# Performance work log

Measured on AMD Instinct MI355X. Metric: run time of the kernel, lower is better.

## Reference

```python
import jax, jax.numpy as jnp
import numpy as np

BN_EPS = 1e-5


def _bn(y, g, b, m, v):
    # BatchNorm1d in eval mode (running stats), faithful to torch's affine BN
    return (y - m) * jax.lax.rsqrt(v + BN_EPS) * g + b


def setup_inputs() -> dict:
    key = jax.random.key(0)
    ks = jax.random.split(key, 6)
    N, E, C_IN, C_OUT = 20000, 640000, 128, 256
    x = jax.random.normal(ks[0], (N, C_IN), dtype=jnp.float32)
    tpl_edge_index = jax.random.randint(ks[1], (2, E), 0, N, dtype=jnp.int64)
    def lin(k, o, i):
        return jax.random.normal(k, (o, i), dtype=jnp.float32) * 0.05
    inp = {
        'x': x,
        'tpl_edge_index': tpl_edge_index,
        'W1': lin(ks[2], C_OUT, 2 * C_IN), 'b1': jnp.zeros((C_OUT,), jnp.float32),
        'g1': jnp.ones((C_OUT,), jnp.float32), 'be1': jnp.zeros((C_OUT,), jnp.float32),
        'm1': jnp.zeros((C_OUT,), jnp.float32), 'v1': jnp.ones((C_OUT,), jnp.float32),
        'W2': lin(ks[3], C_OUT, C_OUT), 'b2': jnp.zeros((C_OUT,), jnp.float32),
        'g2': jnp.ones((C_OUT,), jnp.float32), 'be2': jnp.zeros((C_OUT,), jnp.float32),
        'm2': jnp.zeros((C_OUT,), jnp.float32), 'v2': jnp.ones((C_OUT,), jnp.float32),
        'W3': lin(ks[4], C_OUT, C_OUT), 'b3': jnp.zeros((C_OUT,), jnp.float32),
        'g3': jnp.ones((C_OUT,), jnp.float32), 'be3': jnp.zeros((C_OUT,), jnp.float32),
        'm3': jnp.zeros((C_OUT,), jnp.float32), 'v3': jnp.ones((C_OUT,), jnp.float32),
    }
    return inp


def reference(x, tpl_edge_index, W1, b1, g1, be1, m1, v1,
              W2, b2, g2, be2, m2, v2, W3, b3, g3, be3, m3, v3):
    N = x.shape[0]
    # remove_self_loops + add_self_loops: under max aggregation, duplicate
    # self-loop messages (x_j - x_i == 0) are idempotent, so appending one
    # self-loop per node is mathematically identical.
    loops = jnp.arange(N, dtype=tpl_edge_index.dtype)
    src = jnp.concatenate([tpl_edge_index[0], loops])  # x_j indices
    tgt = jnp.concatenate([tpl_edge_index[1], loops])  # x_i / aggregation indices
    x_i = x[tgt]                                       # [E+N, C_in]
    x_j = x[src]
    h = jnp.concatenate([x_i, x_j - x_i], axis=1)      # [E+N, 2*C_in]
    h = _bn(jax.nn.relu(h @ W1.T + b1), g1, be1, m1, v1)
    h = _bn(jax.nn.relu(h @ W2.T + b2), g2, be2, m2, v2)
    agg = jax.ops.segment_max(h, tgt, num_segments=N)  # scatter-max -> [N, C_out]
    out = _bn(jax.nn.relu(agg @ W3.T + b3), g3, be3, m3, v3)
    return out
```

## Files before the change

### kernel.cpp

```cpp
#include <hip/hip_runtime.h>
#include <stdint.h>

#define BN_EPS 1e-5f

typedef __bf16 bf16x8 __attribute__((ext_vector_type(8)));
typedef __bf16 bf16x2 __attribute__((ext_vector_type(2)));
typedef float  f32x4  __attribute__((ext_vector_type(4)));
typedef float  f32x2  __attribute__((ext_vector_type(2)));

__device__ __forceinline__ unsigned short f2bf(float f) {
    unsigned u = __float_as_uint(f);
    unsigned r = (u + 0x7FFFu + ((u >> 16) & 1u)) >> 16;
    return (unsigned short)r;
}
__device__ __forceinline__ unsigned pkb(float a, float b) {
    f32x2 f; f.x = a; f.y = b;
    bf16x2 h = __builtin_convertvector(f, bf16x2);
    return *(unsigned*)&h;
}
__device__ __forceinline__ unsigned ar2(unsigned p, unsigned q) {
    f32x2 a, b;
    a.x = __uint_as_float(p << 16);
    a.y = __uint_as_float(p & 0xFFFF0000u);
    b.x = __uint_as_float(q << 16);
    b.y = __uint_as_float(q & 0xFFFF0000u);
    f32x2 s = a + b;
    return pkb(fmaxf(s.x, 0.f), fmaxf(s.y, 0.f));
}
__device__ __forceinline__ int swz(int row, int k) {
    const int blk = k >> 3;
    const int sb = (blk & 24) | ((blk ^ row) & 7);
    return (row << 8) + (sb << 3) + (k & 7);
}
__device__ __forceinline__ int swz128(int row, int k) {
    const int blk = k >> 3;
    const int sb = (blk & 8) | ((blk ^ row) & 7);
    return (row << 7) + (sb << 3) + (k & 7);
}

__global__ void prep_kernel(
    const int* __restrict__ eidx,
    int E, int M,
    const float* __restrict__ W1, const float* __restrict__ W2, const float* __restrict__ W3,
    const float* __restrict__ b1, const float* __restrict__ g1, const float* __restrict__ be1,
    const float* __restrict__ m1, const float* __restrict__ v1,
    const float* __restrict__ b2, const float* __restrict__ g2, const float* __restrict__ be2,
    const float* __restrict__ m2, const float* __restrict__ v2,
    const float* __restrict__ b3, const float* __restrict__ g3, const float* __restrict__ be3,
    const float* __restrict__ m3, const float* __restrict__ v3,
    unsigned short* __restrict__ W1b, unsigned short* __restrict__ W2b,
    unsigned short* __restrict__ W3b, float* __restrict__ consts,
    unsigned* __restrict__ mask2, unsigned* __restrict__ count)
{
    const int idx = blockIdx.x * 256 + threadIdx.x;
    if (idx < 65536) {
        const int row = idx >> 8, c = idx & 255;
        float w1v = (c < 128) ? (W1[row * 256 + c] - W1[row * 256 + c + 128])
                              : W1[row * 256 + c];
        W1b[idx] = f2bf(w1v);
        const float s1c = g1[c] * rsqrtf(v1[c] + BN_EPS);
        W2b[idx] = f2bf(W2[idx] * s1c);
        const float s2c = g2[c] * rsqrtf(v2[c] + BN_EPS);
        W3b[idx] = f2bf(W3[idx] * s2c);
    }
    if (idx < 128) {
        const float sa = g2[2 * idx]     * rsqrtf(v2[2 * idx]     + BN_EPS);
        const float sb = g2[2 * idx + 1] * rsqrtf(v2[2 * idx + 1] + BN_EPS);
        mask2[idx] = (sa < 0.f ? 0xFFFFu : 0u) | ((sb < 0.f ? 0xFFFFu : 0u) << 16);
    }
    if (idx < 768) {
        const int l = idx >> 8, c = idx & 255;
        const float* bp  = l == 0 ? b1  : (l == 1 ? b2  : b3);
        const float* gp  = l == 0 ? g1  : (l == 1 ? g2  : g3);
        const float* bep = l == 0 ? be1 : (l == 1 ? be2 : be3);
        const float* mp  = l == 0 ? m1  : (l == 1 ? m2  : m3);
        const float* vp  = l == 0 ? v1  : (l == 1 ? v2  : v3);
        const float s = gp[c] * rsqrtf(vp[c] + BN_EPS);
        consts[l * 768 + c]       = bp[c];
        consts[l * 768 + 256 + c] = s;
        consts[l * 768 + 512 + c] = bep[c] - mp[c] * s;
    }
    if (idx < M) {
        const int tgt = (idx < E) ? eidx[E + idx] : (idx - E);
        atomicAdd(&count[tgt], 1u);
    }
}

__global__ __launch_bounds__(1024) void scan_matvec_kernel(
    const unsigned* __restrict__ count, unsigned* __restrict__ cursor, int N,
    const float* __restrict__ W2, const float* __restrict__ W3,
    float* __restrict__ consts)
{
    const int t = threadIdx.x;
    if (blockIdx.x > 0) {
        const int g = (blockIdx.x - 1) * 16 + (t >> 6);
        const int lane = t & 63;
        const int l = g >> 8, c = g & 255;
        const float* W = l ? W3 : W2;
        const float* tv = consts + (l ? (768 + 512) : 512);
        float4 w4 = *(const float4*)&W[c * 256 + lane * 4];
        float4 t4 = *(const float4*)&tv[lane * 4];
        float s = w4.x * t4.x + w4.y * t4.y + w4.z * t4.z + w4.w * t4.w;
        #pragma unroll
        for (int d = 1; d < 64; d <<= 1) s += __shfl_xor(s, d);
        if (lane == 0) consts[(l ? 1536 : 768) + c] += s;
        return;
    }
    __shared__ unsigned part[1024];
    const int per = (N + 1023) / 1024;
    const int b = t * per;
    unsigned s = 0;
    if (b + per <= N && (per & 3) == 0) {
        for (int i = 0; i < per; i += 4) {
            uint4 c4 = *(const uint4*)(count + b + i);
            s += c4.x + c4.y + c4.z + c4.w;
        }
    } else {
        for (int i = 0; i < per; i++) if (b + i < N) s += count[b + i];
    }
    part[t] = s;
    __syncthreads();
    for (int off = 1; off < 1024; off <<= 1) {
        unsigned v = (t >= off) ? part[t - off] : 0u;
        __syncthreads();
        part[t] += v;
        __syncthreads();
    }
    unsigned run = (t > 0) ? part[t - 1] : 0u;
    for (int i = 0; i < per; i++) {
        if (b + i < N) {
            unsigned c = count[b + i];
            cursor[b + i] = run;
            run += c;
        }
    }
}

__global__ __launch_bounds__(512) void scatpq_kernel(
    const int* __restrict__ eidx, int E, int M, int nScat,
    unsigned* __restrict__ cursor, int* __restrict__ spair,
    const float* __restrict__ x, int N,
    const unsigned short* __restrict__ W1b,
    const float* __restrict__ consts,
    unsigned short* __restrict__ Pb, unsigned short* __restrict__ Qb)
{
    __shared__ unsigned short Xs[64 * 128];
    const int t = threadIdx.x;

    if ((int)blockIdx.x < nScat) {
        const int i = blockIdx.x * 512 + t;
        if (i < M) {
            int s, tg;
            if (i < E) { s = eidx[i]; tg = eidx[E + i]; }
            else       { s = tg = i - E; }
            const unsigned pos = atomicAdd(&cursor[tg], 1u);
            int2* p = (int2*)spair;
            p[pos] = make_int2(s, tg);
        }
        return;
    }

    const int base = (blockIdx.x - nScat) * 64;
    {
        const int row = t >> 3, part = t & 7;
        const int node = base + row;
        const int c0 = part * 16;
        if (node < N) {
            const float* s = x + (size_t)node * 128 + c0;
            float4 a0 = *(const float4*)(s);
            float4 a1 = *(const float4*)(s + 4);
            float4 a2 = *(const float4*)(s + 8);
            float4 a3 = *(const float4*)(s + 12);
            uint4 p0 = {pkb(a0.x, a0.y), pkb(a0.z, a0.w), pkb(a1.x, a1.y), pkb(a1.z, a1.w)};
            uint4 p1 = {pkb(a2.x, a2.y), pkb(a2.z, a2.w), pkb(a3.x, a3.y), pkb(a3.z, a3.w)};
            *(uint4*)&Xs[swz128(row, c0)]     = p0;
            *(uint4*)&Xs[swz128(row, c0 + 8)] = p1;
        } else {
            const uint4 z = {0u, 0u, 0u, 0u};
            *(uint4*)&Xs[swz128(row, c0)]     = z;
            *(uint4*)&Xs[swz128(row, c0 + 8)] = z;
        }
    }
    __syncthreads();

    const int lane = t & 63;
    const int wv   = t >> 6;
    const int n16  = lane & 15;
    const int qd   = lane >> 4;
    const int wc   = wv * 32;

    const f32x4 vzero = {0.f, 0.f, 0.f, 0.f};

    #pragma unroll
    for (int ph = 0; ph < 2; ph++) {
        f32x4 acc[2][4];
        #pragma unroll
        for (int i = 0; i < 2; i++)
            #pragma unroll
            for (int j = 0; j < 4; j++) acc[i][j] = vzero;

        #pragma unroll
        for (int ks = 0; ks < 4; ks++) {
            const int k0 = ks * 32 + qd * 8;
            bf16x8 a[2], b[4];
            #pragma unroll
            for (int ci = 0; ci < 2; ci++)
                a[ci] = *(const bf16x8*)&W1b[(size_t)(wc + ci * 16 + n16) * 256 + ph * 128 + k0];
            #pragma unroll
            for (int rj = 0; rj < 4; rj++)
                b[rj] = *(const bf16x8*)&Xs[swz128(rj * 16 + n16, k0)];
            #pragma unroll
            for (int ci = 0; ci < 2; ci++)
                #pragma unroll
                for (int rj = 0; rj < 4; rj++)
                    acc[ci][rj] = __builtin_amdgcn_mfma_f32_16x16x32_bf16(a[ci], b[rj], acc[ci][rj], 0, 0, 0);
        }

        unsigned short* dst = ph == 0 ? Pb : Qb;
        #pragma unroll
        for (int ci = 0; ci < 2; ci++) {
            const int col0 = wc + ci * 16 + qd * 4;
            float4 bb = {0.f, 0.f, 0.f, 0.f};
            if (ph == 0) bb = *(const float4*)&consts[col0];
            #pragma unroll
            for (int rj = 0; rj < 4; rj++) {
                const int node = base + rj * 16 + n16;
                if (node < N) {
                    uint2 p = {pkb(acc[ci][rj][0] + bb.x, acc[ci][rj][1] + bb.y),
                               pkb(acc[ci][rj][2] + bb.z, acc[ci][rj][3] + bb.w)};
                    *(uint2*)(dst + (size_t)node * 256 + col0) = p;
                }
            }
        }
    }
}

__global__ __launch_bounds__(512) void msg_kernel(
    const unsigned short* __restrict__ Pb,
    const unsigned short* __restrict__ Qb,
    const int* __restrict__ spair,
    int M, int chunk,
    const unsigned short* __restrict__ W2b,
    const float* __restrict__ consts,
    const unsigned* __restrict__ mask2,
    unsigned* __restrict__ agg)
{
    __shared__ unsigned short At[64 * 256];
    __shared__ int tgt_l[64];

    const int tile = (blockIdx.x & 7) * chunk + (blockIdx.x >> 3);
    if (tile * 64 >= M) return;
    const int base = tile * 64;
    const int t = threadIdx.x;

    {
        const int row = t >> 3, part = t & 7;
        const int slot = base + row;
        const int c0 = part * 32;
        if (slot < M) {
            const int2 pr = *(const int2*)(spair + 2 * slot);
            if (part == 0) tgt_l[row] = pr.y;
            const unsigned short* Pp = Pb + (size_t)pr.y * 256 + c0;
            const unsigned short* Qp = Qb + (size_t)pr.x * 256 + c0;
            uint4 P4[4], Q4[4];
            #pragma unroll
            for (int w = 0; w < 4; w++) P4[w] = *(const uint4*)(Pp + w * 8);
            #pragma unroll
            for (int w = 0; w < 4; w++) Q4[w] = *(const uint4*)(Qp + w * 8);
            #pragma unroll
            for (int w = 0; w < 4; w++) {
                uint4 u;
                u.x = ar2(P4[w].x, Q4[w].x);
                u.y = ar2(P4[w].y, Q4[w].y);
                u.z = ar2(P4[w].z, Q4[w].z);
                u.w = ar2(P4[w].w, Q4[w].w);
                *(uint4*)&At[swz(row, c0 + w * 8)] = u;
            }
        } else {
            if (part == 0) tgt_l[row] = -1;
            const uint4 z = {0u, 0u, 0u, 0u};
            #pragma unroll
            for (int w = 0; w < 4; w++) *(uint4*)&At[swz(row, c0 + w * 8)] = z;
        }
    }
    __syncthreads();

    const int lane = t & 63;
    const int wv   = t >> 6;
    const int n16  = lane & 15;
    const int qd   = lane >> 4;
    const int wc   = wv * 32;

    const f32x4 vzero = {0.f, 0.f, 0.f, 0.f};
    f32x4 acc[2][4];
    #pragma unroll
    for (int i = 0; i < 2; i++)
        #pragma unroll
        for (int j = 0; j < 4; j++) acc[i][j] = vzero;

    #pragma unroll
    for (int ks = 0; ks < 8; ks++) {
        const int k0 = ks * 32 + qd * 8;
        bf16x8 a[2], b[4];
        #pragma unroll
        for (int ci = 0; ci < 2; ci++)
            a[ci] = *(const bf16x8*)&W2b[(size_t)(wc + ci * 16 + n16) * 256 + k0];
        #pragma unroll
        for (int rj = 0; rj < 4; rj++)
            b[rj] = *(const bf16x8*)&At[swz(rj * 16 + n16, k0)];
        #pragma unroll
        for (int ci = 0; ci < 2; ci++)
            #pragma unroll
            for (int rj = 0; rj < 4; rj++)
                acc[ci][rj] = __builtin_amdgcn_mfma_f32_16x16x32_bf16(a[ci], b[rj], acc[ci][rj], 0, 0, 0);
    }
    __syncthreads();

    {
        const float* B2 = consts + 768;
        #pragma unroll
        for (int ci = 0; ci < 2; ci++) {
            const int col0 = wc + ci * 16 + qd * 4;
            const float4 bb = *(const float4*)&B2[col0];
            const uint2 mk = *(const uint2*)&mask2[col0 >> 1];
            #pragma unroll
            for (int rj = 0; rj < 4; rj++) {
                const int row = rj * 16 + n16;
                float r0 = fmaxf(acc[ci][rj][0] + bb.x, 0.f);
                float r1 = fmaxf(acc[ci][rj][1] + bb.y, 0.f);
                float r2 = fmaxf(acc[ci][rj][2] + bb.z, 0.f);
                float r3 = fmaxf(acc[ci][rj][3] + bb.w, 0.f);
                uint2 p = {pkb(r0, r1) ^ mk.x, pkb(r2, r3) ^ mk.y};
                *(uint2*)&At[swz(row, col0)] = p;
            }
        }
    }
    __syncthreads();

    {
        const int r0 = (wv & 3) * 16;
        const int cb = (wv >> 2) * 128 + lane * 2;
        const int myt = (lane < 16) ? tgt_l[r0 + lane] : -1;
        int curT = -1;
        unsigned m0 = 0, m1 = 0;
        for (int r = 0; r < 16; r++) {
            const int tg = __shfl(myt, r);
            const unsigned k2 = *(const unsigned*)&At[swz(r0 + r, cb)];
            const unsigned k0 = k2 & 0xFFFFu, k1 = k2 >> 16;
            if (tg != curT) {
                if (curT >= 0) {
                    unsigned* p = &agg[(size_t)curT * 256 + cb];
                    atomicMax(p, m0); atomicMax(p + 1, m1);
                }
                curT = tg; m0 = k0; m1 = k1;
            } else {
                m0 = m0 > k0 ? m0 : k0;
                m1 = m1 > k1 ? m1 : k1;
            }
        }
        if (curT >= 0) {
            unsigned* p = &agg[(size_t)curT * 256 + cb];
            atomicMax(p, m0); atomicMax(p + 1, m1);
        }
    }
}

__global__ __launch_bounds__(256) void out_kernel(
    const unsigned* __restrict__ agg, int N,
    const unsigned short* __restrict__ W3b,
    const float* __restrict__ consts,
    const unsigned* __restrict__ mask2,
    float* __restrict__ out)
{
    __shared__ unsigned short At[32 * 256];

    const int t = threadIdx.x;
    const int base = blockIdx.x * 32;

    {
        const int row = t >> 3, part = t & 7;
        const int node = base + row;
        const int c0 = part * 32;
        if (node < N) {
            const unsigned* ap = agg + (size_t)node * 256 + c0;
            #pragma unroll
            for (int w = 0; w < 4; w++) {
                uint4 a = *(const uint4*)(ap + w * 8);
                uint4 b = *(const uint4*)(ap + w * 8 + 4);
                const uint4 mk = *(const uint4*)&mask2[(c0 + w * 8) >> 1];
                uint4 p;
                p.x = (a.x | (a.y << 16)) ^ mk.x;
                p.y = (a.z | (a.w << 16)) ^ mk.y;
                p.z = (b.x | (b.y << 16)) ^ mk.z;
                p.w = (b.z | (b.w << 16)) ^ mk.w;
                *(uint4*)&At[swz(row, c0 + w * 8)] = p;
            }
        } else {
            const uint4 z = {0u, 0u, 0u, 0u};
            #pragma unroll
            for (int w = 0; w < 4; w++) *(uint4*)&At[swz(row, c0 + w * 8)] = z;
        }
    }
    __syncthreads();

    const int lane = t & 63;
    const int wv   = t >> 6;
    const int n16  = lane & 15;
    const int qd   = lane >> 4;
    const int wc   = wv * 64;

    const f32x4 vzero = {0.f, 0.f, 0.f, 0.f};
    f32x4 acc[2][4];
    #pragma unroll
    for (int i = 0; i < 2; i++)
        #pragma unroll
        for (int j = 0; j < 4; j++) acc[i][j] = vzero;

    #pragma unroll
    for (int ks = 0; ks < 8; ks++) {
        const int k0 = ks * 32 + qd * 8;
        bf16x8 a[2];
        #pragma unroll
        for (int ri = 0; ri < 2; ri++)
            a[ri] = *(const bf16x8*)&At[swz(ri * 16 + n16, k0)];
        #pragma unroll
        for (int ci = 0; ci < 4; ci++) {
            bf16x8 b = *(const bf16x8*)&W3b[(size_t)(wc + ci * 16 + n16) * 256 + k0];
            #pragma unroll
            for (int ri = 0; ri < 2; ri++)
                acc[ri][ci] = __builtin_amdgcn_mfma_f32_16x16x32_bf16(a[ri], b, acc[ri][ci], 0, 0, 0);
        }
    }

    {
        const float* B3 = consts + 1536;
        const float* S3 = consts + 1536 + 256;
        const float* T3 = consts + 1536 + 512;
        #pragma unroll
        for (int ci = 0; ci < 4; ci++) {
            const int col = wc + ci * 16 + n16;
            const float bb = B3[col], ss = S3[col], tt = T3[col];
            #pragma unroll
            for (int ri = 0; ri < 2; ri++) {
                #pragma unroll
                for (int r = 0; r < 4; r++) {
                    const int row = ri * 16 + qd * 4 + r;
                    const int node = base + row;
                    if (node < N) {
                        float v = fmaxf(acc[ri][ci][r] + bb, 0.f) * ss + tt;
                        out[(size_t)node * 256 + col] = v;
                    }
                }
            }
        }
    }
}

extern "C" void kernel_launch(void* const* d_in, const int* in_sizes, int n_in,
                              void* d_out, int out_size, void* d_ws, size_t ws_size,
                              hipStream_t stream)
{
    const float* x  = (const float*)d_in[0];
    const int* eidx = (const int*)d_in[1];
    const int N = in_sizes[0] / 128;
    const int E = in_sizes[1] / 2;
    const int M = E + N;
    const int nTiles = (M + 63) / 64;
    const int chunk = (nTiles + 7) / 8;
    const int nScat = (M + 511) / 512;
    const int nPQ = (N + 63) / 64;

    char* ws = (char*)d_ws;
    unsigned short* W1b = (unsigned short*)(ws);
    unsigned short* W2b = (unsigned short*)(ws + 131072);
    unsigned short* W3b = (unsigned short*)(ws + 262144);
    float* consts       = (float*)(ws + 393216);
    unsigned* mask2     = (unsigned*)(ws + 402432);
    size_t off = 402944;
    unsigned* agg       = (unsigned*)(ws + off);       off += (size_t)N * 256 * 4;
    unsigned* count     = (unsigned*)(ws + off);       off += (size_t)N * 4;
    unsigned* cursor    = (unsigned*)(ws + off);       off += (size_t)N * 4;
    int* spair          = (int*)(ws + off);            off += (size_t)M * 8;
    unsigned short* Pb  = (unsigned short*)(ws + off); off += (size_t)N * 256 * 2;
    unsigned short* Qb  = (unsigned short*)(ws + off);

    hipMemsetAsync(agg, 0, (size_t)N * 256 * 4, stream);
    hipMemsetAsync(count, 0, (size_t)N * 4, stream);

    int work = M;
    if (65536 > work) work = 65536;
    hipLaunchKernelGGL(prep_kernel, dim3((work + 255) / 256), dim3(256), 0, stream,
        eidx, E, M,
        (const float*)d_in[2], (const float*)d_in[8], (const float*)d_in[14],
        (const float*)d_in[3], (const float*)d_in[4], (const float*)d_in[5],
        (const float*)d_in[6], (const float*)d_in[7],
        (const float*)d_in[9], (const float*)d_in[10], (const float*)d_in[11],
        (const float*)d_in[12], (const float*)d_in[13],
        (const float*)d_in[15], (const float*)d_in[16], (const float*)d_in[17],
        (const float*)d_in[18], (const float*)d_in[19],
        W1b, W2b, W3b, consts, mask2, count);

    hipLaunchKernelGGL(scan_matvec_kernel, dim3(33), dim3(1024), 0, stream,
        count, cursor, N,
        (const float*)d_in[8], (const float*)d_in[14], consts);

    hipLaunchKernelGGL(scatpq_kernel, dim3(nScat + nPQ), dim3(512), 0, stream,
        eidx, E, M, nScat, cursor, spair,
        x, N, W1b, consts, Pb, Qb);

    hipLaunchKernelGGL(msg_kernel, dim3(chunk * 8), dim3(512), 0, stream,
        Pb, Qb, spair, M, chunk, W2b, consts, mask2, agg);

    hipLaunchKernelGGL(out_kernel, dim3((N + 31) / 32), dim3(256), 0, stream,
        agg, N, W3b, consts, mask2, (float*)d_out);
}
```

Baseline: 471.6 us.

## Use per-wave LDS epilogue tiles to drop block barriers; fold agg zeroing into prep

The msg_kernel epilogue now writes each wave's 64x32 output slice into a private swizzled LDS buffer and performs the segment-max scan on that slice itself, removing two block-wide __syncthreads. Each lane handles one column pair across 16 rows, with four row groups per wave. Zeroing of the aggregation buffer moves from a separate hipMemsetAsync into a grid-stride loop inside prep_kernel, saving one launch. The costs are about 32KB of extra LDS per block, which may lower occupancy, and a different atomic pattern: runs break per quarter-wave, so more atomics may be issued.

```diff
diff --git a/kernel.cpp b/kernel.cpp
--- a/kernel.cpp
+++ b/kernel.cpp
@@ -36,6 +36,10 @@
     const int blk = k >> 3;
     const int sb = (blk & 8) | ((blk ^ row) & 7);
     return (row << 7) + (sb << 3) + (k & 7);
+}
+__device__ __forceinline__ int swz32(int row, int c) {
+    const int cc = c ^ (((row ^ (row >> 3)) & 7) << 2);
+    return (row << 5) + cc;
 }
 
 __global__ void prep_kernel(
@@ -50,7 +54,8 @@
     const float* __restrict__ m3, const float* __restrict__ v3,
     unsigned short* __restrict__ W1b, unsigned short* __restrict__ W2b,
     unsigned short* __restrict__ W3b, float* __restrict__ consts,
-    unsigned* __restrict__ mask2, unsigned* __restrict__ count)
+    unsigned* __restrict__ mask2, unsigned* __restrict__ count,
+    unsigned* __restrict__ agg, int aggWords)
 {
     const int idx = blockIdx.x * 256 + threadIdx.x;
     if (idx < 65536) {
@@ -83,6 +88,12 @@
     if (idx < M) {
         const int tgt = (idx < E) ? eidx[E + idx] : (idx - E);
         atomicAdd(&count[tgt], 1u);
+    }
+    {
+        const uint4 z = {0u, 0u, 0u, 0u};
+        const int stride = gridDim.x * 256 * 4;
+        for (int i = idx * 4; i < aggWords; i += stride)
+            *(uint4*)&agg[i] = z;
     }
 }
 
@@ -246,6 +257,7 @@
     unsigned* __restrict__ agg)
 {
     __shared__ unsigned short At[64 * 256];
+    __shared__ unsigned short Kt[8][64 * 32];
     __shared__ int tgt_l[64];
 
     const int tile = (blockIdx.x & 7) * chunk + (blockIdx.x >> 3);
@@ -314,13 +326,14 @@
             for (int rj = 0; rj < 4; rj++)
                 acc[ci][rj] = __builtin_amdgcn_mfma_f32_16x16x32_bf16(a[ci], b[rj], acc[ci][rj], 0, 0, 0);
     }
-    __syncthreads();
-
+
+    unsigned short* K = Kt[wv];
     {
         const float* B2 = consts + 768;
         #pragma unroll
         for (int ci = 0; ci < 2; ci++) {
-            const int col0 = wc + ci * 16 + qd * 4;
+            const int cl = ci * 16 + qd * 4;
+            const int col0 = wc + cl;
             const float4 bb = *(const float4*)&B2[col0];
             const uint2 mk = *(const uint2*)&mask2[col0 >> 1];
             #pragma unroll
@@ -331,25 +344,25 @@
                 float r2 = fmaxf(acc[ci][rj][2] + bb.z, 0.f);
                 float r3 = fmaxf(acc[ci][rj][3] + bb.w, 0.f);
                 uint2 p = {pkb(r0, r1) ^ mk.x, pkb(r2, r3) ^ mk.y};
-                *(uint2*)&At[swz(row, col0)] = p;
+                *(uint2*)&K[swz32(row, cl)] = p;
             }
         }
     }
-    __syncthreads();
-
-    {
-        const int r0 = (wv & 3) * 16;
-        const int cb = (wv >> 2) * 128 + lane * 2;
-        const int myt = (lane < 16) ? tgt_l[r0 + lane] : -1;
+
+    {
+        const int cp = lane & 15;
+        const int q  = lane >> 4;
+        const int myt = tgt_l[lane];
         int curT = -1;
         unsigned m0 = 0, m1 = 0;
-        for (int r = 0; r < 16; r++) {
-            const int tg = __shfl(myt, r);
-            const unsigned k2 = *(const unsigned*)&At[swz(r0 + r, cb)];
+        for (int j = 0; j < 16; j++) {
+            const int row = q * 16 + j;
+            const int tg = __shfl(myt, row);
+            const unsigned k2 = *(const unsigned*)&K[swz32(row, cp * 2)];
             const unsigned k0 = k2 & 0xFFFFu, k1 = k2 >> 16;
             if (tg != curT) {
                 if (curT >= 0) {
-                    unsigned* p = &agg[(size_t)curT * 256 + cb];
+                    unsigned* p = &agg[(size_t)curT * 256 + wc + cp * 2];
                     atomicMax(p, m0); atomicMax(p + 1, m1);
                 }
                 curT = tg; m0 = k0; m1 = k1;
@@ -359,7 +372,7 @@
             }
         }
         if (curT >= 0) {
-            unsigned* p = &agg[(size_t)curT * 256 + cb];
+            unsigned* p = &agg[(size_t)curT * 256 + wc + cp * 2];
             atomicMax(p, m0); atomicMax(p + 1, m1);
         }
     }
@@ -484,7 +497,6 @@
     unsigned short* Pb  = (unsigned short*)(ws + off); off += (size_t)N * 256 * 2;
     unsigned short* Qb  = (unsigned short*)(ws + off);
 
-    hipMemsetAsync(agg, 0, (size_t)N * 256 * 4, stream);
     hipMemsetAsync(count, 0, (size_t)N * 4, stream);
 
     int work = M;
@@ -498,7 +510,7 @@
         (const float*)d_in[12], (const float*)d_in[13],
         (const float*)d_in[15], (const float*)d_in[16], (const float*)d_in[17],
         (const float*)d_in[18], (const float*)d_in[19],
-        W1b, W2b, W3b, consts, mask2, count);
+        W1b, W2b, W3b, consts, mask2, count, agg, N * 256);
 
     hipLaunchKernelGGL(scan_matvec_kernel, dim3(33), dim3(1024), 0, stream,
         count, cursor, N,
```

Measured after the change: 478.2 us. About the same (+1.4%).
